# Kernel optimization log

Hardware: AMD Instinct MI355X
Metric: run time of the kernel (lower is better)

## Reference

```python
import jax, jax.numpy as jnp
import numpy as np

VOCAB = 100  # hardcoded in the torch module


def setup_inputs() -> dict:
    key = jax.random.key(0)
    ks = jax.random.split(key, 8)
    T, B = 128, 1024
    M, Dq, Dv = 32, 64, 64
    questions = jax.random.randint(ks[0], (T, B), 0, VOCAB, dtype=jnp.int32)
    answers = jax.random.randint(ks[1], (T, B), 0, VOCAB, dtype=jnp.int32)
    Eq = jax.random.normal(ks[2], (VOCAB, Dq), dtype=jnp.float32)
    Ev = jax.random.normal(ks[3], (VOCAB, Dv), dtype=jnp.float32)
    Wa = jax.random.normal(ks[4], (Dq, M), dtype=jnp.float32) / np.sqrt(Dq)
    ba = jnp.zeros((M,), dtype=jnp.float32)
    Wf = jax.random.normal(ks[5], (Dq + Dv, 1), dtype=jnp.float32) / np.sqrt(Dq + Dv)
    bf = jnp.zeros((1,), dtype=jnp.float32)
    return {"questions": questions, "answers": answers, "Eq": Eq, "Ev": Ev,
            "Wa": Wa, "ba": ba, "Wf": Wf, "bf": bf}


def reference(questions, answers, Eq, Ev, Wa, ba, Wf, bf):
    T, B = questions.shape
    M = Wa.shape[1]
    Dv = Ev.shape[1]

    # Per-timestep quantities independent of memory state: compute vectorized.
    q_embed = Eq[questions]                                   # (T, B, Dq)
    att = jax.nn.softmax(q_embed @ Wa + ba, axis=-1)          # (T, B, M)
    write_idx = (questions * 2 + answers) % VOCAB             # (T, B)
    qa_embed = Ev[write_idx]                                  # (T, B, Dv)

    # Split fc weight for concat([q_embed, read]) @ Wf.
    Dq = Eq.shape[1]
    Wf_q, Wf_r = Wf[:Dq], Wf[Dq:]                             # (Dq,1), (Dv,1)

    mem0 = jnp.zeros((B, M, Dv), dtype=q_embed.dtype)

    def step(mem, inputs):
        q_t, att_t, qa_t = inputs                             # (B,Dq),(B,M),(B,Dv)
        read = jnp.einsum('bm,bmd->bd', att_t, mem)           # (B, Dv)
        pred = (q_t @ Wf_q + read @ Wf_r)[:, 0] + bf[0]       # (B,)
        mem = mem + jnp.einsum('bm,bd->bmd', att_t, qa_t)     # outer-product write
        return mem, pred

    _, preds = jax.lax.scan(step, mem0, (q_embed, att, qa_embed))
    return preds                                              # (T, B)
```

## Files before the change

kernel.cpp:

```cpp
#include <hip/hip_runtime.h>
#include <math.h>

#define VOCAB 100
#define TT    128
#define BB    1024
#define MM    32
#define DQ    64
#define DV    64
#define BPB   8
#define NTHR  256
#define CH    32
#define NCH   (TT / CH)
#define PSTR  34

__global__ __launch_bounds__(NTHR) void dkvmn_fused(
    const int* __restrict__ questions,
    const int* __restrict__ answers,
    const float* __restrict__ Eq,
    const float* __restrict__ Ev,
    const float* __restrict__ Wa,
    const float* __restrict__ ba,
    const float* __restrict__ Wf,
    const float* __restrict__ bf,
    float* __restrict__ out) {

  __shared__ float att_l[VOCAB * MM];
  __shared__ float sq_l[VOCAB];
  __shared__ float sv_l[VOCAB];
  __shared__ __align__(16) float wf_l[2 * DQ + 1];
  __shared__ __align__(16) float2 qsv_l[BPB * TT];
  __shared__ float pred_l[TT * 9 + 8];
  __shared__ __align__(16) float big[BPB * MM * PSTR];

  const int tid = threadIdx.x;
  const int b0  = blockIdx.x * BPB;
  const int g   = tid >> 5;
  const int m   = tid & 31;

  {
    const float4* Eq4 = (const float4*)Eq;
    float4* dst = (float4*)big;
    #pragma unroll
    for (int it = 0; it < 7; ++it) {
      int i = tid + it * NTHR;
      if (i < VOCAB * DQ / 4) dst[i] = Eq4[i];
    }
  }
  if (tid < 2 * DQ) wf_l[tid] = Wf[tid];
  if (tid == NTHR - 1) wf_l[2 * DQ] = bf[0];

  #pragma unroll
  for (int it = 0; it < 4; ++it) {
    int idx = tid + it * NTHR;
    int t = idx >> 3, j = idx & 7;
    int gi = t * BB + b0 + j;
    int q = questions[gi];
    int a = answers[gi];
    int w = (q * 2 + a) % VOCAB;
    qsv_l[j * TT + t] = make_float2(__int_as_float(q), __int_as_float(w));
  }

  float wa[DQ];
  #pragma unroll
  for (int k = 0; k < DQ; ++k) wa[k] = Wa[k * MM + m];
  const float bam = ba[m];

  __syncthreads();

  for (int q = g; q < VOCAB; q += BPB) {
    const float4* eq4 = (const float4*)(big + q * DQ);
    float ax = 0.f, ay = 0.f, az = 0.f, aw = 0.f;
    #pragma unroll
    for (int k4 = 0; k4 < DQ / 4; ++k4) {
      float4 e = eq4[k4];
      ax = fmaf(e.x, wa[k4 * 4 + 0], ax);
      ay = fmaf(e.y, wa[k4 * 4 + 1], ay);
      az = fmaf(e.z, wa[k4 * 4 + 2], az);
      aw = fmaf(e.w, wa[k4 * 4 + 3], aw);
    }
    float l = (ax + ay) + (az + aw) + bam;
    float mx = l;
    #pragma unroll
    for (int k = 16; k >= 1; k >>= 1) mx = fmaxf(mx, __shfl_xor(mx, k));
    float ex = __expf(l - mx);
    float sm = ex;
    #pragma unroll
    for (int k = 16; k >= 1; k >>= 1) sm += __shfl_xor(sm, k);
    att_l[q * MM + m] = ex * __builtin_amdgcn_rcpf(sm);
  }

  if (tid < VOCAB) {
    const float4* eq4 = (const float4*)(big + tid * DQ);
    const float4* wfq = (const float4*)wf_l;
    float s = 0.f;
    #pragma unroll
    for (int k4 = 0; k4 < DQ / 4; ++k4) {
      float4 e = eq4[k4], w = wfq[k4];
      s = fmaf(e.x, w.x, fmaf(e.y, w.y, fmaf(e.z, w.z, fmaf(e.w, w.w, s))));
    }
    sq_l[tid] = s + wf_l[2 * DQ];
  } else if (tid >= 128 && tid < 128 + VOCAB) {
    int v = tid - 128;
    const float4* ev4 = (const float4*)Ev + v * (DV / 4);
    const float4* wfr = (const float4*)(wf_l + DQ);
    float s = 0.f;
    #pragma unroll
    for (int k4 = 0; k4 < DV / 4; ++k4) {
      float4 e = ev4[k4], w = wfr[k4];
      s = fmaf(e.x, w.x, fmaf(e.y, w.y, fmaf(e.z, w.z, fmaf(e.w, w.w, s))));
    }
    sv_l[v] = s;
  }

  __syncthreads();

  #pragma unroll
  for (int it = 0; it < 4; ++it) {
    int idx = tid + it * NTHR;
    int t = idx >> 3, j = idx & 7;
    float2 x = qsv_l[j * TT + t];
    x.y = sv_l[__float_as_int(x.y)];
    qsv_l[j * TT + t] = x;
  }
  __syncthreads();

  float rvec = 0.f;
  const float2* qsv_g = qsv_l + g * TT;
  float* pacc = big + g * (MM * PSTR);

  for (int c = 0; c < NCH; ++c) {
    const float4* x4 = (const float4*)(qsv_g + c * CH);
    #pragma unroll
    for (int h = 0; h < CH / 2; ++h) {
      float4 x = x4[h];
      int q0 = __float_as_int(x.x);
      float av0 = att_l[q0 * MM + m];
      float p0 = av0 * rvec;
      rvec = fmaf(av0, x.y, rvec);
      int q1 = __float_as_int(x.z);
      float av1 = att_l[q1 * MM + m];
      float p1 = av1 * rvec;
      rvec = fmaf(av1, x.w, rvec);
      *(float2*)(pacc + m * PSTR + 2 * h) = make_float2(p0, p1);
    }
    float s = 0.f;
    #pragma unroll
    for (int k = 0; k < MM; ++k) s += pacc[k * PSTR + m];
    int t = c * CH + m;
    int q = __float_as_int(qsv_g[t].x);
    pred_l[t * 9 + g] = s + sq_l[q];
  }

  __syncthreads();

  {
    int t = tid >> 1, h = tid & 1;
    float4 v;
    v.x = pred_l[t * 9 + h * 4 + 0];
    v.y = pred_l[t * 9 + h * 4 + 1];
    v.z = pred_l[t * 9 + h * 4 + 2];
    v.w = pred_l[t * 9 + h * 4 + 3];
    *(float4*)(out + t * BB + b0 + h * 4) = v;
  }
}

extern "C" void kernel_launch(void* const* d_in, const int* in_sizes, int n_in,
                              void* d_out, int out_size, void* d_ws, size_t ws_size,
                              hipStream_t stream) {
  const int*   questions = (const int*)d_in[0];
  const int*   answers   = (const int*)d_in[1];
  const float* Eq = (const float*)d_in[2];
  const float* Ev = (const float*)d_in[3];
  const float* Wa = (const float*)d_in[4];
  const float* ba = (const float*)d_in[5];
  const float* Wf = (const float*)d_in[6];
  const float* bf = (const float*)d_in[7];
  float* out = (float*)d_out;

  hipLaunchKernelGGL(dkvmn_fused, dim3(BB / BPB), dim3(NTHR), 0, stream,
                     questions, answers, Eq, Ev, Wa, ba, Wf, bf, out);
}
```

Before: 20.11 us.

## Split attention logits across LDS/global sources, per-row softmax, direct output stores

Half the warps now read Eq rows straight from global memory while the other half read them from LDS, which spreads the load across two paths. Each warp writes raw logits into a padded attention table, and a separate pass has one thread per vocab row do the softmax, replacing the shuffle reductions. The partial-product buffer is transposed so the reduction can use float4 row reads. The pred staging buffer and the final barrier are removed, and each lane writes its prediction to global directly. In exchange it adds one more barrier, makes the global stores uncoalesced (stride BB between lanes), and gives the softmax pass serial per-thread work.

```diff
diff --git a/kernel.cpp b/kernel.cpp
--- a/kernel.cpp
+++ b/kernel.cpp
@@ -11,7 +11,8 @@
 #define NTHR  256
 #define CH    32
 #define NCH   (TT / CH)
-#define PSTR  34
+#define ASTR  36
+#define PSTR  36
 
 __global__ __launch_bounds__(NTHR) void dkvmn_fused(
     const int* __restrict__ questions,
@@ -24,13 +25,12 @@
     const float* __restrict__ bf,
     float* __restrict__ out) {
 
-  __shared__ float att_l[VOCAB * MM];
+  __shared__ __align__(16) float att_l[VOCAB * ASTR];
   __shared__ float sq_l[VOCAB];
   __shared__ float sv_l[VOCAB];
   __shared__ __align__(16) float wf_l[2 * DQ + 1];
   __shared__ __align__(16) float2 qsv_l[BPB * TT];
-  __shared__ float pred_l[TT * 9 + 8];
-  __shared__ __align__(16) float big[BPB * MM * PSTR];
+  __shared__ __align__(16) float big[BPB * CH * PSTR];
 
   const int tid = threadIdx.x;
   const int b0  = blockIdx.x * BPB;
@@ -67,30 +67,64 @@
 
   __syncthreads();
 
-  for (int q = g; q < VOCAB; q += BPB) {
-    const float4* eq4 = (const float4*)(big + q * DQ);
-    float ax = 0.f, ay = 0.f, az = 0.f, aw = 0.f;
-    #pragma unroll
-    for (int k4 = 0; k4 < DQ / 4; ++k4) {
-      float4 e = eq4[k4];
-      ax = fmaf(e.x, wa[k4 * 4 + 0], ax);
-      ay = fmaf(e.y, wa[k4 * 4 + 1], ay);
-      az = fmaf(e.z, wa[k4 * 4 + 2], az);
-      aw = fmaf(e.w, wa[k4 * 4 + 3], aw);
-    }
-    float l = (ax + ay) + (az + aw) + bam;
-    float mx = l;
-    #pragma unroll
-    for (int k = 16; k >= 1; k >>= 1) mx = fmaxf(mx, __shfl_xor(mx, k));
-    float ex = __expf(l - mx);
-    float sm = ex;
-    #pragma unroll
-    for (int k = 16; k >= 1; k >>= 1) sm += __shfl_xor(sm, k);
-    att_l[q * MM + m] = ex * __builtin_amdgcn_rcpf(sm);
-  }
-
-  if (tid < VOCAB) {
-    const float4* eq4 = (const float4*)(big + tid * DQ);
+  if ((tid >> 6) & 1) {
+    for (int q = g; q < VOCAB; q += BPB) {
+      const float4* eq4 = (const float4*)(Eq + q * DQ);
+      float ax = 0.f, ay = 0.f, az = 0.f, aw = 0.f;
+      #pragma unroll
+      for (int k4 = 0; k4 < DQ / 4; ++k4) {
+        float4 e = eq4[k4];
+        ax = fmaf(e.x, wa[4 * k4 + 0], ax);
+        ay = fmaf(e.y, wa[4 * k4 + 1], ay);
+        az = fmaf(e.z, wa[4 * k4 + 2], az);
+        aw = fmaf(e.w, wa[4 * k4 + 3], aw);
+      }
+      att_l[q * ASTR + m] = (ax + ay) + (az + aw) + bam;
+    }
+  } else {
+    for (int q = g; q < VOCAB; q += BPB) {
+      const float4* eq4 = (const float4*)(big + q * DQ);
+      float ax = 0.f, ay = 0.f, az = 0.f, aw = 0.f;
+      #pragma unroll
+      for (int k4 = 0; k4 < DQ / 4; ++k4) {
+        float4 e = eq4[k4];
+        ax = fmaf(e.x, wa[4 * k4 + 0], ax);
+        ay = fmaf(e.y, wa[4 * k4 + 1], ay);
+        az = fmaf(e.z, wa[4 * k4 + 2], az);
+        aw = fmaf(e.w, wa[4 * k4 + 3], aw);
+      }
+      att_l[q * ASTR + m] = (ax + ay) + (az + aw) + bam;
+    }
+  }
+
+  __syncthreads();
+
+  if (tid < 128) {
+    if (tid < VOCAB) {
+      const int q = tid;
+      float4* row = (float4*)(att_l + q * ASTR);
+      float v[MM];
+      #pragma unroll
+      for (int j = 0; j < 8; ++j) {
+        float4 x = row[j];
+        v[4 * j + 0] = x.x; v[4 * j + 1] = x.y;
+        v[4 * j + 2] = x.z; v[4 * j + 3] = x.w;
+      }
+      float mx = v[0];
+      #pragma unroll
+      for (int k = 1; k < MM; ++k) mx = fmaxf(mx, v[k]);
+      float sm = 0.f;
+      #pragma unroll
+      for (int k = 0; k < MM; ++k) { v[k] = __expf(v[k] - mx); sm += v[k]; }
+      const float inv = __builtin_amdgcn_rcpf(sm);
+      #pragma unroll
+      for (int j = 0; j < 8; ++j)
+        row[j] = make_float4(v[4 * j + 0] * inv, v[4 * j + 1] * inv,
+                             v[4 * j + 2] * inv, v[4 * j + 3] * inv);
+    }
+  } else if (tid - 128 < VOCAB) {
+    const int v = tid - 128;
+    const float4* eq4 = (const float4*)(big + v * DQ);
     const float4* wfq = (const float4*)wf_l;
     float s = 0.f;
     #pragma unroll
@@ -98,18 +132,16 @@
       float4 e = eq4[k4], w = wfq[k4];
       s = fmaf(e.x, w.x, fmaf(e.y, w.y, fmaf(e.z, w.z, fmaf(e.w, w.w, s))));
     }
-    sq_l[tid] = s + wf_l[2 * DQ];
-  } else if (tid >= 128 && tid < 128 + VOCAB) {
-    int v = tid - 128;
+    sq_l[v] = s + wf_l[2 * DQ];
     const float4* ev4 = (const float4*)Ev + v * (DV / 4);
     const float4* wfr = (const float4*)(wf_l + DQ);
-    float s = 0.f;
+    float s2 = 0.f;
     #pragma unroll
     for (int k4 = 0; k4 < DV / 4; ++k4) {
       float4 e = ev4[k4], w = wfr[k4];
-      s = fmaf(e.x, w.x, fmaf(e.y, w.y, fmaf(e.z, w.z, fmaf(e.w, w.w, s))));
-    }
-    sv_l[v] = s;
+      s2 = fmaf(e.x, w.x, fmaf(e.y, w.y, fmaf(e.z, w.z, fmaf(e.w, w.w, s2))));
+    }
+    sv_l[v] = s2;
   }
 
   __syncthreads();
@@ -126,7 +158,7 @@
 
   float rvec = 0.f;
   const float2* qsv_g = qsv_l + g * TT;
-  float* pacc = big + g * (MM * PSTR);
+  float* pacc = big + g * (CH * PSTR);
 
   for (int c = 0; c < NCH; ++c) {
     const float4* x4 = (const float4*)(qsv_g + c * CH);
@@ -134,33 +166,24 @@
     for (int h = 0; h < CH / 2; ++h) {
       float4 x = x4[h];
       int q0 = __float_as_int(x.x);
-      float av0 = att_l[q0 * MM + m];
-      float p0 = av0 * rvec;
+      float av0 = att_l[q0 * ASTR + m];
+      pacc[(2 * h + 0) * PSTR + m] = av0 * rvec;
       rvec = fmaf(av0, x.y, rvec);
       int q1 = __float_as_int(x.z);
-      float av1 = att_l[q1 * MM + m];
-      float p1 = av1 * rvec;
+      float av1 = att_l[q1 * ASTR + m];
+      pacc[(2 * h + 1) * PSTR + m] = av1 * rvec;
       rvec = fmaf(av1, x.w, rvec);
-      *(float2*)(pacc + m * PSTR + 2 * h) = make_float2(p0, p1);
-    }
+    }
+    const float4* prow = (const float4*)(pacc + m * PSTR);
     float s = 0.f;
     #pragma unroll
-    for (int k = 0; k < MM; ++k) s += pacc[k * PSTR + m];
+    for (int j = 0; j < 8; ++j) {
+      float4 r = prow[j];
+      s += (r.x + r.y) + (r.z + r.w);
+    }
     int t = c * CH + m;
     int q = __float_as_int(qsv_g[t].x);
-    pred_l[t * 9 + g] = s + sq_l[q];
-  }
-
-  __syncthreads();
-
-  {
-    int t = tid >> 1, h = tid & 1;
-    float4 v;
-    v.x = pred_l[t * 9 + h * 4 + 0];
-    v.y = pred_l[t * 9 + h * 4 + 1];
-    v.z = pred_l[t * 9 + h * 4 + 2];
-    v.w = pred_l[t * 9 + h * 4 + 3];
-    *(float4*)(out + t * BB + b0 + h * 4) = v;
+    out[t * BB + b0 + g] = s + sq_l[q];
   }
 }
 
```

After: 17.01 us. 15.4% less time.
